# Kernel tuning notes

Measured on AMD Instinct MI355X. Metric: run time of the kernel, lower is better.

## Reference

```python
import jax, jax.numpy as jnp
import numpy as np

N_EMBD = 1024
HEAD_SIZE = 64  # n_embd // n_head = 1024 // 16


def setup_inputs() -> dict:
    key = jax.random.key(0)
    ks = jax.random.split(key, 7)
    B, T, C, H = 4, 2048, N_EMBD, HEAD_SIZE
    s = 1.0 / np.sqrt(C)
    return {
        "x": jax.random.normal(ks[0], (B, T, C), dtype=jnp.float32),
        "Wq": jax.random.normal(ks[1], (C, H), dtype=jnp.float32) * s,
        "bq": jax.random.normal(ks[2], (H,), dtype=jnp.float32) * 0.01,
        "Wk": jax.random.normal(ks[3], (C, H), dtype=jnp.float32) * s,
        "bk": jax.random.normal(ks[4], (H,), dtype=jnp.float32) * 0.01,
        "Wv": jax.random.normal(ks[5], (C, H), dtype=jnp.float32) * s,
        "bv": jax.random.normal(ks[6], (H,), dtype=jnp.float32) * 0.01,
    }


def reference(x, Wq, bq, Wk, bk, Wv, bv):
    # x: [B, T, C]
    B, T, C = x.shape
    q = x @ Wq + bq  # [B, T, H]
    k = x @ Wk + bk  # [B, T, H]
    v = x @ Wv + bv  # [B, T, H]
    # NOTE: original module does NOT scale by 1/sqrt(head_size)
    wei = jnp.einsum("bth,bsh->bts", q, k)  # [B, T, T]
    causal = jnp.tril(jnp.ones((T, T), dtype=bool))
    wei = jnp.where(causal, wei, -jnp.inf)
    wei = jax.nn.softmax(wei, axis=-1)
    out = jnp.einsum("bts,bsh->bth", wei, v)  # [B, T, H]
    return out
```

## Files before the change

### kernel.cpp

```cpp
#include <hip/hip_runtime.h>

typedef float f32x4 __attribute__((ext_vector_type(4)));
typedef short s16x4 __attribute__((ext_vector_type(4)));
typedef short s16x8 __attribute__((ext_vector_type(8)));

#define LOG2E 1.4426950408889634f

__device__ __forceinline__ short f2bf(float f) {
  unsigned u = __float_as_uint(f);
  unsigned r = (u + 0x7fffu + ((u >> 16) & 1u)) >> 16;
  return (short)r;
}
__device__ __forceinline__ float bf2f(short s) {
  return __uint_as_float(((unsigned)(unsigned short)s) << 16);
}

__device__ __forceinline__ f32x4 mfma16(s16x4 a, s16x4 b, f32x4 c) {
  return __builtin_amdgcn_mfma_f32_16x16x16bf16_1k(a, b, c, 0, 0, 0);
}
__device__ __forceinline__ f32x4 mfma32(s16x8 a, s16x8 b, f32x4 c) {
  return __builtin_amdgcn_mfma_f32_16x16x32_bf16(a, b, c, 0, 0, 0);
}

__device__ __forceinline__ void gl_lds16(const void* gp, void* sp) {
  __builtin_amdgcn_global_load_lds(
      (__attribute__((address_space(1))) void*)const_cast<void*>(gp),
      (__attribute__((address_space(3))) void*)sp, 16, 0, 0);
}

__global__ __launch_bounds__(256) void prep_w(
    const float* __restrict__ Wq, const float* __restrict__ Wk, const float* __restrict__ Wv,
    short* __restrict__ wt_hi, short* __restrict__ wt_lo) {
  int idx = blockIdx.x * 256 + threadIdx.x;
  int n = idx >> 10;
  int c = idx & 1023;
  const float* W = (n < 64) ? Wq : ((n < 128) ? Wk : Wv);
  float v = W[c * 64 + (n & 63)];
  short hi = f2bf(v);
  short lo = f2bf(v - bf2f(hi));
  wt_hi[idx] = hi;
  wt_lo[idx] = lo;
}

__global__ __launch_bounds__(512, 2) void proj_qkv(
    const float* __restrict__ x,
    const short* __restrict__ wt_hi, const short* __restrict__ wt_lo,
    const float* __restrict__ bq, const float* __restrict__ bk, const float* __restrict__ bv,
    short* __restrict__ q_hi, short* __restrict__ q_lo,
    short* __restrict__ k_hi, short* __restrict__ k_lo,
    short* __restrict__ v_t) {
  const int tid = threadIdx.x;
  const int lane = tid & 63;
  const int wv = tid >> 6;
  const int col = lane & 15;
  const int g = lane >> 4;
  const int mg = wv >> 2;
  const int ng = wv & 3;
  const int tokbase = blockIdx.x * 32;

  __shared__ short lds[3][24576];

  const int arow = mg * 16 + col;
  const int qrow = ng * 16 + col;
  const int krow = 64 + ng * 16 + col;
  const int vrow = 128 + ng * 16 + col;

  f32x4 accQ = {0,0,0,0}, accK = {0,0,0,0}, accV = {0,0,0,0};

#define STAGE(bp, s) do { \
    _Pragma("unroll") \
    for (int j = 0; j < 5; ++j) { \
      const int c_ = wv + 8 * j; \
      const short* src_; short* dst_; \
      if (c_ < 24) { \
        const int r_ = c_ * 8 + (lane >> 3); \
        const int lc_ = (lane & 7) ^ (r_ & 7); \
        src_ = wt_hi + (size_t)r_ * 1024 + (s) * 64 + lc_ * 8; \
        dst_ = (bp) + c_ * 512; \
      } else { \
        const int r_ = (c_ - 24) * 8 + (lane >> 3); \
        const int lc_ = (lane & 7) ^ (r_ & 7); \
        src_ = wt_lo + (size_t)r_ * 1024 + (s) * 64 + lc_ * 8; \
        dst_ = (bp) + 12288 + (c_ - 24) * 512; \
      } \
      gl_lds16(src_, dst_); \
    } \
    { \
      const int r_ = wv * 4 + (lane >> 4); \
      const int lc_ = (lane & 15) ^ (r_ & 15); \
      const float* xs_ = x + (size_t)(tokbase + r_) * 1024 + (s) * 64 + lc_ * 4; \
      float* xd_ = (float*)((bp) + 20480) + wv * 256; \
      gl_lds16(xs_, xd_); \
    } \
  } while (0)

#define PIPE_WAIT(N) do { \
    asm volatile("s_waitcnt vmcnt(" #N ")" ::: "memory"); \
    __builtin_amdgcn_s_barrier(); \
    __builtin_amdgcn_sched_barrier(0); \
  } while (0)
#define PIPE_END do { \
    asm volatile("s_waitcnt lgkmcnt(0)" ::: "memory"); \
    __builtin_amdgcn_sched_barrier(0); \
    __builtin_amdgcn_s_barrier(); \
  } while (0)

#define COMPUTE(bp) do { \
    const short* wb_ = (bp); \
    const float* xb_ = (const float*)((bp) + 20480); \
    _Pragma("unroll") \
    for (int h = 0; h < 2; ++h) { \
      const int hc_ = h * 8 + g * 2; \
      f32x4 x0_ = *(const f32x4*)(xb_ + arow * 64 + ((hc_       ^ (arow & 15)) << 2)); \
      f32x4 x1_ = *(const f32x4*)(xb_ + arow * 64 + (((hc_ + 1) ^ (arow & 15)) << 2)); \
      s16x8 xh_, xl_; \
      _Pragma("unroll") for (int i = 0; i < 4; ++i) { \
        short t0_ = f2bf(x0_[i]); xh_[i] = t0_; xl_[i] = f2bf(x0_[i] - bf2f(t0_)); \
        short t1_ = f2bf(x1_[i]); xh_[4 + i] = t1_; xl_[4 + i] = f2bf(x1_[i] - bf2f(t1_)); \
      } \
      const int wc_ = h * 4 + g; \
      s16x8 qh_ = *(const s16x8*)(wb_ + qrow * 64 + ((wc_ ^ (qrow & 7)) << 3)); \
      s16x8 kh_ = *(const s16x8*)(wb_ + krow * 64 + ((wc_ ^ (krow & 7)) << 3)); \
      s16x8 vh_ = *(const s16x8*)(wb_ + vrow * 64 + ((wc_ ^ (vrow & 7)) << 3)); \
      s16x8 ql_ = *(const s16x8*)(wb_ + 12288 + qrow * 64 + ((wc_ ^ (qrow & 7)) << 3)); \
      s16x8 kl_ = *(const s16x8*)(wb_ + 12288 + krow * 64 + ((wc_ ^ (krow & 7)) << 3)); \
      accQ = mfma32(xh_, qh_, accQ); \
      accK = mfma32(xh_, kh_, accK); \
      accV = mfma32(xh_, vh_, accV); \
      accQ = mfma32(xl_, qh_, accQ); \
      accK = mfma32(xl_, kh_, accK); \
      accQ = mfma32(xh_, ql_, accQ); \
      accK = mfma32(xh_, kl_, accK); \
    } \
  } while (0)

  short* b0 = &lds[0][0];
  short* b1 = &lds[1][0];
  short* b2 = &lds[2][0];

  STAGE(b0, 0);
  STAGE(b1, 1);
#pragma unroll 1
  for (int s = 0; s < 12; s += 3) {
    STAGE(b2, s + 2); PIPE_WAIT(6); COMPUTE(b0); PIPE_END;
    STAGE(b0, s + 3); PIPE_WAIT(6); COMPUTE(b1); PIPE_END;
    STAGE(b1, s + 4); PIPE_WAIT(6); COMPUTE(b2); PIPE_END;
  }
  STAGE(b2, 14); PIPE_WAIT(6); COMPUTE(b0); PIPE_END;
  STAGE(b0, 15); PIPE_WAIT(6); COMPUTE(b1); PIPE_END;
  PIPE_WAIT(3);  COMPUTE(b2); PIPE_END;
  PIPE_WAIT(0);  COMPUTE(b0); PIPE_END;

  {
    const int hQ = ng * 16 + col;
    const float biasq = bq[hQ];
    const float biask = bk[hQ];
    const float biasv = bv[hQ];
#pragma unroll
    for (int r = 0; r < 4; ++r) {
      const int tok = tokbase + mg * 16 + 4 * g + r;
      float fq = accQ[r] + biasq;
      short qh = f2bf(fq);
      q_hi[(size_t)tok * 64 + hQ] = qh;
      q_lo[(size_t)tok * 64 + hQ] = f2bf(fq - bf2f(qh));
      float fk = accK[r] + biask;
      short kh = f2bf(fk);
      k_hi[(size_t)tok * 64 + hQ] = kh;
      k_lo[(size_t)tok * 64 + hQ] = f2bf(fk - bf2f(kh));
      const int bb = tok >> 11;
      const int tl = tok & 2047;
      v_t[((size_t)bb * 64 + hQ) * 2048 + tl] = f2bf(accV[r] + biasv);
    }
  }
#undef STAGE
#undef COMPUTE
}

__global__ __launch_bounds__(512, 2) void attn(
    const short* __restrict__ q_hi, const short* __restrict__ q_lo,
    const short* __restrict__ k_hi, const short* __restrict__ k_lo,
    const short* __restrict__ v_t,
    float* __restrict__ pm, float* __restrict__ pl, float* __restrict__ pO) {
  const int tid = threadIdx.x;
  const int lane = tid & 63;
  const int w = tid >> 6;
  const int col = lane & 15;
  const int g = lane >> 4;
  const int bid = blockIdx.x;
  const int p = bid & 7;
  const int b = (bid >> 3) & 3;
  const int s = bid >> 5;
  if (s > p) return;

  __shared__ short lds[3][12288];

  const int qlo = 256 * p + 32 * w;
  const int kb0 = 256 * s;

  const short* qbh = q_hi + (size_t)(b * 2048 + qlo + col) * 64 + g * 8;
  const short* qbl = q_lo + (size_t)(b * 2048 + qlo + col) * 64 + g * 8;
  s16x8 qh0a = *(const s16x8*)(qbh);
  s16x8 qh1a = *(const s16x8*)(qbh + 32);
  s16x8 ql0a = *(const s16x8*)(qbl);
  s16x8 ql1a = *(const s16x8*)(qbl + 32);
  s16x8 qh0b = *(const s16x8*)(qbh + 16 * 64);
  s16x8 qh1b = *(const s16x8*)(qbh + 16 * 64 + 32);
  s16x8 ql0b = *(const s16x8*)(qbl + 16 * 64);
  s16x8 ql1b = *(const s16x8*)(qbl + 16 * 64 + 32);
  asm volatile("s_waitcnt vmcnt(0)" ::: "memory");
  __builtin_amdgcn_sched_barrier(0);

  f32x4 oA0 = {0,0,0,0}, oA1 = {0,0,0,0}, oA2 = {0,0,0,0}, oA3 = {0,0,0,0};
  f32x4 oB0 = {0,0,0,0}, oB1 = {0,0,0,0}, oB2 = {0,0,0,0}, oB3 = {0,0,0,0};
  float mA = -3.0e38f, lA = 0.0f, mB = -3.0e38f, lB = 0.0f;
  const f32x4 NEGV = {-3.0e38f, -3.0e38f, -3.0e38f, -3.0e38f};

#define STAGE(BP, J) do { \
    const int kbs_ = kb0 + 64 * (J); \
    const int r_ = 8 * w + (lane >> 3); \
    const int lc_ = (lane & 7) ^ (lane >> 3); \
    gl_lds16(k_hi + (size_t)(b * 2048 + kbs_ + r_) * 64 + lc_ * 8, (BP) + 8 * w * 64); \
    gl_lds16(k_lo + (size_t)(b * 2048 + kbs_ + r_) * 64 + lc_ * 8, (BP) + 4096 + 8 * w * 64); \
    gl_lds16(v_t + ((size_t)b * 64 + r_) * 2048 + kbs_ + lc_ * 8, (BP) + 8192 + 8 * w * 64); \
  } while (0)

#define PIPE_WAIT(N) do { \
    asm volatile("s_waitcnt vmcnt(" #N ")" ::: "memory"); \
    __builtin_amdgcn_s_barrier(); \
    __builtin_amdgcn_sched_barrier(0); \
  } while (0)
#define PIPE_END do { \
    asm volatile("s_waitcnt lgkmcnt(0)" ::: "memory"); \
    __builtin_amdgcn_sched_barrier(0); \
    __builtin_amdgcn_s_barrier(); \
  } while (0)

#define QK_U(U) do { \
    const int kg0_ = kb_ + 16 * U; \
    if (kg0_ <= qlo + 31) { \
      const short* kr_ = bp_ + (16 * U + col) * 64; \
      const int cx_ = col & 7; \
      s16x8 kh0_ = *(const s16x8*)(kr_ + ((g ^ cx_) << 3)); \
      s16x8 kh1_ = *(const s16x8*)(kr_ + (((4 + g) ^ cx_) << 3)); \
      s16x8 kl0_ = *(const s16x8*)(kr_ + 4096 + ((g ^ cx_) << 3)); \
      s16x8 kl1_ = *(const s16x8*)(kr_ + 4096 + (((4 + g) ^ cx_) << 3)); \
      if (kg0_ <= qlo + 15) { \
        f32x4 u1_ = {0,0,0,0}, u2_ = {0,0,0,0}; \
        u1_ = mfma32(kh0_, qh0a, u1_); u1_ = mfma32(kh1_, qh1a, u1_); \
        u2_ = mfma32(kh0_, ql0a, u2_); u2_ = mfma32(kh1_, ql1a, u2_); \
        u2_ = mfma32(kl0_, qh0a, u2_); u2_ = mfma32(kl1_, qh1a, u2_); \
        scA##U = u1_ + u2_; \
        if (kg0_ == qlo) { \
          _Pragma("unroll") for (int i = 0; i < 4; ++i) \
            if (4 * g + i > col) scA##U[i] = -3.0e38f; \
        } \
      } \
      { \
        f32x4 u1_ = {0,0,0,0}, u2_ = {0,0,0,0}; \
        u1_ = mfma32(kh0_, qh0b, u1_); u1_ = mfma32(kh1_, qh1b, u1_); \
        u2_ = mfma32(kh0_, ql0b, u2_); u2_ = mfma32(kh1_, ql1b, u2_); \
        u2_ = mfma32(kl0_, qh0b, u2_); u2_ = mfma32(kl1_, qh1b, u2_); \
        scB##U = u1_ + u2_; \
        if (kg0_ == qlo + 16) { \
          _Pragma("unroll") for (int i = 0; i < 4; ++i) \
            if (4 * g + i > col) scB##U[i] = -3.0e38f; \
        } \
      } \
    } \
  } while (0)

#define SMAX4(v) fmaxf(fmaxf((v)[0], (v)[1]), fmaxf((v)[2], (v)[3]))

#define SOFTMAX_X(s0v, s1v, s2v, s3v, mX, lX, o0X, o1X, o2X, o3X, p0X, p1X, p2X, p3X) do { \
    float mx_ = fmaxf(fmaxf(SMAX4(s0v), SMAX4(s1v)), fmaxf(SMAX4(s2v), SMAX4(s3v))); \
    mx_ = fmaxf(mx_, __shfl_xor(mx_, 16)); \
    mx_ = fmaxf(mx_, __shfl_xor(mx_, 32)); \
    const float mn_ = fmaxf(mX, mx_); \
    const float rs_ = __builtin_amdgcn_exp2f((mX - mn_) * LOG2E); \
    float ls_ = 0.f; \
    _Pragma("unroll") for (int i = 0; i < 4; ++i) { \
      float e0_ = __builtin_amdgcn_exp2f((s0v[i] - mn_) * LOG2E); \
      float e1_ = __builtin_amdgcn_exp2f((s1v[i] - mn_) * LOG2E); \
      float e2_ = __builtin_amdgcn_exp2f((s2v[i] - mn_) * LOG2E); \
      float e3_ = __builtin_amdgcn_exp2f((s3v[i] - mn_) * LOG2E); \
      p0X[i] = f2bf(e0_); p1X[i] = f2bf(e1_); p2X[i] = f2bf(e2_); p3X[i] = f2bf(e3_); \
      ls_ += e0_ + e1_ + e2_ + e3_; \
    } \
    lX = lX * rs_ + ls_; \
    o0X *= rs_; o1X *= rs_; o2X *= rs_; o3X *= rs_; \
    mX = mn_; \
  } while (0)

#define PV_U(U) do { \
    const int kg0_ = kb_ + 16 * U; \
    if (kg0_ <= qlo + 31) { \
      const int cx_ = col & 7; \
      const short* vr_ = bp_ + 8192 + col * 64 + ((g & 1) << 2) + \
                         (((2 * U + (g >> 1)) ^ cx_) << 3); \
      s16x4 v0_ = *(const s16x4*)(vr_); \
      s16x4 v1_ = *(const s16x4*)(vr_ + 1024); \
      s16x4 v2_ = *(const s16x4*)(vr_ + 2048); \
      s16x4 v3_ = *(const s16x4*)(vr_ + 3072); \
      if (kg0_ <= qlo + 15) { \
        oA0 = mfma16(v0_, pbA##U, oA0); \
        oA1 = mfma16(v1_, pbA##U, oA1); \
        oA2 = mfma16(v2_, pbA##U, oA2); \
        oA3 = mfma16(v3_, pbA##U, oA3); \
      } \
      oB0 = mfma16(v0_, pbB##U, oB0); \
      oB1 = mfma16(v1_, pbB##U, oB1); \
      oB2 = mfma16(v2_, pbB##U, oB2); \
      oB3 = mfma16(v3_, pbB##U, oB3); \
    } \
  } while (0)

#define COMPUTE(BP, J) do { \
    const int kb_ = kb0 + 64 * (J); \
    if (kb_ <= qlo + 31) { \
      const short* bp_ = (BP); \
      f32x4 scA0 = NEGV, scA1 = NEGV, scA2 = NEGV, scA3 = NEGV; \
      f32x4 scB0 = NEGV, scB1 = NEGV, scB2 = NEGV, scB3 = NEGV; \
      QK_U(0); QK_U(1); QK_U(2); QK_U(3); \
      s16x4 pbA0, pbA1, pbA2, pbA3, pbB0, pbB1, pbB2, pbB3; \
      if (kb_ <= qlo + 15) \
        SOFTMAX_X(scA0, scA1, scA2, scA3, mA, lA, oA0, oA1, oA2, oA3, \
                  pbA0, pbA1, pbA2, pbA3); \
      SOFTMAX_X(scB0, scB1, scB2, scB3, mB, lB, oB0, oB1, oB2, oB3, \
                pbB0, pbB1, pbB2, pbB3); \
      PV_U(0); PV_U(1); PV_U(2); PV_U(3); \
    } \
  } while (0)

  short* L0 = &lds[0][0];
  short* L1 = &lds[1][0];
  short* L2 = &lds[2][0];

  STAGE(L0, 0); STAGE(L1, 1);
  STAGE(L2, 2); PIPE_WAIT(6); COMPUTE(L0, 0); PIPE_END;
  STAGE(L0, 3); PIPE_WAIT(6); COMPUTE(L1, 1); PIPE_END;
  PIPE_WAIT(3); COMPUTE(L2, 2); PIPE_END;
  PIPE_WAIT(0); COMPUTE(L0, 3);

  lA += __shfl_xor(lA, 16); lA += __shfl_xor(lA, 32);
  lB += __shfl_xor(lB, 16); lB += __shfl_xor(lB, 32);
  const int rowA = b * 2048 + qlo + col;
  const int rowB = rowA + 16;
  if (g == 0) {
    pm[s * 8192 + rowA] = mA;  pl[s * 8192 + rowA] = lA;
    pm[s * 8192 + rowB] = mB;  pl[s * 8192 + rowB] = lB;
  }
  {
    float* dA = pO + ((size_t)s * 8192 + rowA) * 64 + 4 * g;
    float* dB = pO + ((size_t)s * 8192 + rowB) * 64 + 4 * g;
    *(f32x4*)(dA)      = oA0; *(f32x4*)(dA + 16) = oA1;
    *(f32x4*)(dA + 32) = oA2; *(f32x4*)(dA + 48) = oA3;
    *(f32x4*)(dB)      = oB0; *(f32x4*)(dB + 16) = oB1;
    *(f32x4*)(dB + 32) = oB2; *(f32x4*)(dB + 48) = oB3;
  }
#undef STAGE
#undef PIPE_WAIT
#undef PIPE_END
#undef QK_U
#undef SMAX4
#undef SOFTMAX_X
#undef PV_U
#undef COMPUTE
}

__global__ __launch_bounds__(256) void reduce_p(
    const float* __restrict__ pm, const float* __restrict__ pl,
    const float* __restrict__ pO, float* __restrict__ out) {
  const int idx = blockIdx.x * 256 + threadIdx.x;
  const int row = idx >> 4;
  const int hq = (idx & 15) * 4;
  const int smax = (row & 2047) >> 8;
  float M = -3.0e38f;
  for (int s = 0; s <= smax; ++s) M = fmaxf(M, pm[s * 8192 + row]);
  float L = 0.f;
  f32x4 acc = {0, 0, 0, 0};
  for (int s = 0; s <= smax; ++s) {
    const float ws = __builtin_amdgcn_exp2f((pm[s * 8192 + row] - M) * LOG2E);
    L += ws * pl[s * 8192 + row];
    f32x4 ov = *(const f32x4*)(pO + ((size_t)s * 8192 + row) * 64 + hq);
    acc += ov * ws;
  }
  const float invL = 1.0f / L;
  *(f32x4*)(out + (size_t)row * 64 + hq) = acc * invL;
}

extern "C" void kernel_launch(void* const* d_in, const int* in_sizes, int n_in,
                              void* d_out, int out_size, void* d_ws, size_t ws_size,
                              hipStream_t stream) {
  const float* x  = (const float*)d_in[0];
  const float* Wq = (const float*)d_in[1];
  const float* bq = (const float*)d_in[2];
  const float* Wk = (const float*)d_in[3];
  const float* bk = (const float*)d_in[4];
  const float* Wv = (const float*)d_in[5];
  const float* bv = (const float*)d_in[6];
  float* out = (float*)d_out;

  char* ws = (char*)d_ws;
  short* wt_hi = (short*)(ws);
  short* wt_lo = (short*)(ws + 393216);
  short* q_hi  = (short*)(ws + 786432);
  short* q_lo  = (short*)(ws + 786432 + 1048576);
  short* k_hi  = (short*)(ws + 786432 + 2 * 1048576);
  short* k_lo  = (short*)(ws + 786432 + 3 * 1048576);
  short* v_t   = (short*)(ws + 786432 + 4 * 1048576);
  float* pm    = (float*)(ws + 6029312);
  float* pl    = (float*)(ws + 6291456);
  float* pO    = (float*)(ws + 6553600);

  hipLaunchKernelGGL(prep_w, dim3(768), dim3(256), 0, stream, Wq, Wk, Wv, wt_hi, wt_lo);
  hipLaunchKernelGGL(proj_qkv, dim3(256), dim3(512), 0, stream,
                     x, wt_hi, wt_lo, bq, bk, bv, q_hi, q_lo, k_hi, k_lo, v_t);
  hipLaunchKernelGGL(attn, dim3(256), dim3(512), 0, stream,
                     q_hi, q_lo, k_hi, k_lo, v_t, pm, pl, pO);
  hipLaunchKernelGGL(reduce_p, dim3(512), dim3(256), 0, stream, pm, pl, pO, out);
}
```

Baseline: 56.03 us.

## Deepen QKV projection pipeline to five smaller stages with packed bf16 conversion

The projection kernel's K-loop changes from a triple-buffered 64-wide step to a five-buffer ring of 32-wide steps. Four stages stay in flight, and staging is precomputed into three async global-to-LDS loads per thread with a new swizzle. The hi/lo bf16 split of x now uses the packed v_cvt_pk_bf16_f32 instruction instead of manual rounding. The aim is better hiding of global load latency and fewer VALU instructions. In exchange there are twice as many barriers and iterations, and the hardware conversion may round differently from the old software rounding.

```diff
diff --git a/kernel.cpp b/kernel.cpp
--- a/kernel.cpp
+++ b/kernel.cpp
@@ -13,6 +13,11 @@
 }
 __device__ __forceinline__ float bf2f(short s) {
   return __uint_as_float(((unsigned)(unsigned short)s) << 16);
+}
+__device__ __forceinline__ unsigned cvt_pk_bf16(float a, float b) {
+  unsigned r;
+  asm("v_cvt_pk_bf16_f32 %0, %1, %2" : "=v"(r) : "v"(a), "v"(b));
+  return r;
 }
 
 __device__ __forceinline__ f32x4 mfma16(s16x4 a, s16x4 b, f32x4 c) {
@@ -58,40 +63,28 @@
   const int ng = wv & 3;
   const int tokbase = blockIdx.x * 32;
 
-  __shared__ short lds[3][24576];
-
-  const int arow = mg * 16 + col;
-  const int qrow = ng * 16 + col;
-  const int krow = 64 + ng * 16 + col;
-  const int vrow = 128 + ng * 16 + col;
-
-  f32x4 accQ = {0,0,0,0}, accK = {0,0,0,0}, accV = {0,0,0,0};
-
-#define STAGE(bp, s) do { \
-    _Pragma("unroll") \
-    for (int j = 0; j < 5; ++j) { \
-      const int c_ = wv + 8 * j; \
-      const short* src_; short* dst_; \
-      if (c_ < 24) { \
-        const int r_ = c_ * 8 + (lane >> 3); \
-        const int lc_ = (lane & 7) ^ (r_ & 7); \
-        src_ = wt_hi + (size_t)r_ * 1024 + (s) * 64 + lc_ * 8; \
-        dst_ = (bp) + c_ * 512; \
-      } else { \
-        const int r_ = (c_ - 24) * 8 + (lane >> 3); \
-        const int lc_ = (lane & 7) ^ (r_ & 7); \
-        src_ = wt_lo + (size_t)r_ * 1024 + (s) * 64 + lc_ * 8; \
-        dst_ = (bp) + 12288 + (c_ - 24) * 512; \
-      } \
-      gl_lds16(src_, dst_); \
-    } \
-    { \
-      const int r_ = wv * 4 + (lane >> 4); \
-      const int lc_ = (lane & 15) ^ (r_ & 15); \
-      const float* xs_ = x + (size_t)(tokbase + r_) * 1024 + (s) * 64 + lc_ * 4; \
-      float* xd_ = (float*)((bp) + 20480) + wv * 256; \
-      gl_lds16(xs_, xd_); \
-    } \
+  __shared__ short lds[5][12288];
+
+  const int wsl = ((lane & 3) ^ ((lane >> 3) & 3)) * 8;
+  const short* s0 = wt_hi + (size_t)(16 * wv + (lane >> 2)) * 1024 + wsl;
+  const int d0 = wv * 512;
+  const int c1 = wv + 8;
+  const short* s1 = (c1 < 12 ? wt_hi + (size_t)(16 * c1 + (lane >> 2)) * 1024
+                             : wt_lo + (size_t)(16 * (c1 - 12) + (lane >> 2)) * 1024) + wsl;
+  const int d1 = (c1 < 12) ? c1 * 512 : 6144 + (c1 - 12) * 512;
+  const int c2 = wv + 16;
+  const bool isx = (c2 >= 20);
+  const short* s2 = isx
+      ? (const short*)(x + (size_t)(tokbase + 8 * (c2 - 20) + (lane >> 3)) * 1024 +
+                       ((lane & 7) ^ (lane >> 3)) * 4)
+      : wt_lo + (size_t)(16 * (c2 - 12) + (lane >> 2)) * 1024 + wsl;
+  const int d2 = isx ? 10240 + (c2 - 20) * 512 : 6144 + (c2 - 12) * 512;
+  const int st2 = isx ? 64 : 32;
+
+#define STAGE(BP, S) do { \
+    gl_lds16(s0 + (S) * 32, (BP) + d0); \
+    gl_lds16(s1 + (S) * 32, (BP) + d1); \
+    gl_lds16(s2 + (S) * st2, (BP) + d2); \
   } while (0)
 
 #define PIPE_WAIT(N) do { \
@@ -105,51 +98,68 @@
     __builtin_amdgcn_s_barrier(); \
   } while (0)
 
-#define COMPUTE(bp) do { \
-    const short* wb_ = (bp); \
-    const float* xb_ = (const float*)((bp) + 20480); \
-    _Pragma("unroll") \
-    for (int h = 0; h < 2; ++h) { \
-      const int hc_ = h * 8 + g * 2; \
-      f32x4 x0_ = *(const f32x4*)(xb_ + arow * 64 + ((hc_       ^ (arow & 15)) << 2)); \
-      f32x4 x1_ = *(const f32x4*)(xb_ + arow * 64 + (((hc_ + 1) ^ (arow & 15)) << 2)); \
-      s16x8 xh_, xl_; \
-      _Pragma("unroll") for (int i = 0; i < 4; ++i) { \
-        short t0_ = f2bf(x0_[i]); xh_[i] = t0_; xl_[i] = f2bf(x0_[i] - bf2f(t0_)); \
-        short t1_ = f2bf(x1_[i]); xh_[4 + i] = t1_; xl_[4 + i] = f2bf(x1_[i] - bf2f(t1_)); \
-      } \
-      const int wc_ = h * 4 + g; \
-      s16x8 qh_ = *(const s16x8*)(wb_ + qrow * 64 + ((wc_ ^ (qrow & 7)) << 3)); \
-      s16x8 kh_ = *(const s16x8*)(wb_ + krow * 64 + ((wc_ ^ (krow & 7)) << 3)); \
-      s16x8 vh_ = *(const s16x8*)(wb_ + vrow * 64 + ((wc_ ^ (vrow & 7)) << 3)); \
-      s16x8 ql_ = *(const s16x8*)(wb_ + 12288 + qrow * 64 + ((wc_ ^ (qrow & 7)) << 3)); \
-      s16x8 kl_ = *(const s16x8*)(wb_ + 12288 + krow * 64 + ((wc_ ^ (krow & 7)) << 3)); \
-      accQ = mfma32(xh_, qh_, accQ); \
-      accK = mfma32(xh_, kh_, accK); \
-      accV = mfma32(xh_, vh_, accV); \
-      accQ = mfma32(xl_, qh_, accQ); \
-      accK = mfma32(xl_, kh_, accK); \
-      accQ = mfma32(xh_, ql_, accQ); \
-      accK = mfma32(xh_, kl_, accK); \
-    } \
-  } while (0)
-
-  short* b0 = &lds[0][0];
-  short* b1 = &lds[1][0];
-  short* b2 = &lds[2][0];
-
-  STAGE(b0, 0);
-  STAGE(b1, 1);
+  const int arow = mg * 16 + col;
+  const int xq0 = ((2 * g) ^ (arow & 7)) << 2;
+  const int xq1 = ((2 * g + 1) ^ (arow & 7)) << 2;
+  const int rq = ng * 16 + col;
+  const int ws = (g ^ ((rq >> 1) & 3)) << 3;
+
+  f32x4 accQ = {0,0,0,0}, accK = {0,0,0,0}, accV = {0,0,0,0};
+
+  typedef union { unsigned u[4]; s16x8 v8; } pk8;
+
+#define COMPUTE(BP) do { \
+    const short* bp_ = (BP); \
+    const float* xb_ = (const float*)(bp_ + 10240); \
+    f32x4 x0_ = *(const f32x4*)(xb_ + arow * 32 + xq0); \
+    f32x4 x1_ = *(const f32x4*)(xb_ + arow * 32 + xq1); \
+    pk8 xh_, xl_; \
+    xh_.u[0] = cvt_pk_bf16(x0_[0], x0_[1]); \
+    xh_.u[1] = cvt_pk_bf16(x0_[2], x0_[3]); \
+    xh_.u[2] = cvt_pk_bf16(x1_[0], x1_[1]); \
+    xh_.u[3] = cvt_pk_bf16(x1_[2], x1_[3]); \
+    xl_.u[0] = cvt_pk_bf16(x0_[0] - __uint_as_float(xh_.u[0] << 16), \
+                           x0_[1] - __uint_as_float(xh_.u[0] & 0xffff0000u)); \
+    xl_.u[1] = cvt_pk_bf16(x0_[2] - __uint_as_float(xh_.u[1] << 16), \
+                           x0_[3] - __uint_as_float(xh_.u[1] & 0xffff0000u)); \
+    xl_.u[2] = cvt_pk_bf16(x1_[0] - __uint_as_float(xh_.u[2] << 16), \
+                           x1_[1] - __uint_as_float(xh_.u[2] & 0xffff0000u)); \
+    xl_.u[3] = cvt_pk_bf16(x1_[2] - __uint_as_float(xh_.u[3] << 16), \
+                           x1_[3] - __uint_as_float(xh_.u[3] & 0xffff0000u)); \
+    s16x8 qh_ = *(const s16x8*)(bp_ + rq * 32 + ws); \
+    s16x8 kh_ = *(const s16x8*)(bp_ + (64 + rq) * 32 + ws); \
+    s16x8 vh_ = *(const s16x8*)(bp_ + (128 + rq) * 32 + ws); \
+    s16x8 ql_ = *(const s16x8*)(bp_ + 6144 + rq * 32 + ws); \
+    s16x8 kl_ = *(const s16x8*)(bp_ + 6144 + (64 + rq) * 32 + ws); \
+    accQ = mfma32(xh_.v8, qh_, accQ); \
+    accK = mfma32(xh_.v8, kh_, accK); \
+    accV = mfma32(xh_.v8, vh_, accV); \
+    accQ = mfma32(xl_.v8, qh_, accQ); \
+    accK = mfma32(xl_.v8, kh_, accK); \
+    accQ = mfma32(xh_.v8, ql_, accQ); \
+    accK = mfma32(xh_.v8, kl_, accK); \
+  } while (0)
+
+  short* cA = &lds[0][0];
+  short* cB = &lds[1][0];
+  short* cC = &lds[2][0];
+  short* cD = &lds[3][0];
+  short* cE = &lds[4][0];
+
+  STAGE(cA, 0); STAGE(cB, 1); STAGE(cC, 2); STAGE(cD, 3);
+
 #pragma unroll 1
-  for (int s = 0; s < 12; s += 3) {
-    STAGE(b2, s + 2); PIPE_WAIT(6); COMPUTE(b0); PIPE_END;
-    STAGE(b0, s + 3); PIPE_WAIT(6); COMPUTE(b1); PIPE_END;
-    STAGE(b1, s + 4); PIPE_WAIT(6); COMPUTE(b2); PIPE_END;
+  for (int b = 0; b < 28; ++b) {
+    STAGE(cE, b + 4);
+    PIPE_WAIT(12);
+    COMPUTE(cA);
+    PIPE_END;
+    short* t = cA; cA = cB; cB = cC; cC = cD; cD = cE; cE = t;
   }
-  STAGE(b2, 14); PIPE_WAIT(6); COMPUTE(b0); PIPE_END;
-  STAGE(b0, 15); PIPE_WAIT(6); COMPUTE(b1); PIPE_END;
-  PIPE_WAIT(3);  COMPUTE(b2); PIPE_END;
-  PIPE_WAIT(0);  COMPUTE(b0); PIPE_END;
+  PIPE_WAIT(9); COMPUTE(cA); PIPE_END;
+  PIPE_WAIT(6); COMPUTE(cB); PIPE_END;
+  PIPE_WAIT(3); COMPUTE(cC); PIPE_END;
+  PIPE_WAIT(0); COMPUTE(cD);
 
   {
     const int hQ = ng * 16 + col;
@@ -173,6 +183,8 @@
     }
   }
 #undef STAGE
+#undef PIPE_WAIT
+#undef PIPE_END
 #undef COMPUTE
 }
 
```

Result: no change. 55.42 us (-1.1%).
